# Optimization experiments

Hardware: AMD Instinct MI355X
Metric: run time of the kernel (lower is better)

## Reference

```python
import jax, jax.numpy as jnp
import numpy as np

R = 2  # upsample factor (init kwarg r)


def _cheby1_sos(N, rp, Wn):
    """Pure-numpy replication of scipy.signal.cheby1(N, rp, Wn, 'lowpass', output='sos')
    for even N (all-pole lowpass). Pairing of conjugate poles may differ from scipy's
    zpk2sos ordering but the cascaded transfer function is identical (same poles,
    zeros all at z=-1, same overall gain)."""
    # analog Chebyshev-I prototype (scipy.cheb1ap)
    eps = np.sqrt(10.0 ** (0.1 * rp) - 1.0)
    mu = np.arcsinh(1.0 / eps) / N
    m = np.arange(-N + 1, N, 2)
    theta = np.pi * m / (2.0 * N)
    p = -np.sinh(mu + 1j * theta)
    k = np.prod(-p).real
    if N % 2 == 0:
        k /= np.sqrt(1.0 + eps * eps)
    # pre-warp (fs = 2) and lowpass scale (lp2lp_zpk)
    fs = 2.0
    warped = 2.0 * fs * np.tan(np.pi * Wn / fs)
    p = p * warped
    k = k * warped ** N
    # bilinear transform (bilinear_zpk); zeros -> -1 with multiplicity N
    fs2 = 2.0 * fs
    pz = (fs2 + p) / (fs2 - p)
    kz = k * np.real(1.0 / np.prod(fs2 - p))
    # build SOS: each conjugate pole pair gets two zeros at -1
    pos = pz[np.imag(pz) > 0]  # N//2 poles in upper half plane
    sos = np.zeros((N // 2, 6), dtype=np.float64)
    for i, pp in enumerate(pos):
        sos[i, 0:3] = [1.0, 2.0, 1.0]                      # b: (1 + z^-1)^2
        sos[i, 3:6] = [1.0, -2.0 * pp.real, abs(pp) ** 2]  # a
    sos[0, 0:3] *= kz  # fold overall gain into first section
    return sos


_SOS = _cheby1_sos(8, 0.05, 1.0 / R)  # [4, 6], a0 == 1


def _biquad(x, b0, b1, b2, a1, a2):
    # x: [B, T]; transposed direct-form-II biquad, matching torchaudio's
    def step(carry, xt):
        z1, z2 = carry
        y = b0 * xt + z1
        z1n = b1 * xt - a1 * y + z2
        z2n = b2 * xt - a2 * y
        return (z1n, z2n), y

    B = x.shape[0]
    init = (jnp.zeros((B,), x.dtype), jnp.zeros((B,), x.dtype))
    _, y = jax.lax.scan(step, init, x.T)  # scan over time
    return y.T


def setup_inputs() -> dict:
    key = jax.random.key(0)
    x = jax.random.normal(key, (256, 32768), dtype=jnp.float32)
    return {"x": x}


def reference(x):
    *lead, T = x.shape
    xb = x.reshape(-1, T)
    up = jnp.repeat(xb, R, axis=-1)        # nearest-neighbor upsample by R
    y = up[:, ::-1]                        # flip(-1)
    for row in _SOS:                       # 4 cascaded biquad sections
        b0, b1, b2, a0, a1, a2 = [float(v) for v in row]
        y = _biquad(y, b0 / a0, b1 / a0, b2 / a0, a1 / a0, a2 / a0)
    y = y[:, ::-1]                         # flip back
    return y.reshape(*lead, T * R)
```

## Files before the change

### kernel.cpp

```cpp
#include <hip/hip_runtime.h>
#include <cmath>
#include <complex>


struct KArgs {
  float g;
  float a1[4];
  float a2[4];
  float w[64][8];
};

struct G2 { float4 a, b; };

#define SWZ(q) ((q) ^ ((((q) >> 6) & 7) << 2))

__global__ __launch_bounds__(64)
void cheby_up_kernel(const float* __restrict__ x, float* __restrict__ y, KArgs c) {
  constexpr int T_IN = 32768;
  constexpr int TILE = 2048;
  __shared__ __align__(16) float lbuf[TILE + 64];

  const int row = blockIdx.x >> 4;
  const int tb  = blockIdx.x & 15;
  const int l   = threadIdx.x;
  const float* xrow = x + (size_t)row * T_IN;
  float*       yrow = y + (size_t)row * (size_t)(2 * T_IN);
  const int tbase = TILE * tb;

  const float g = c.g;

  #pragma unroll
  for (int j = 0; j < 8; ++j) {
    int q = 4 * l + 256 * j;
    float4 v = *reinterpret_cast<const float4*>(xrow + tbase + q);
    v.x *= g; v.y *= g; v.z *= g; v.w *= g;
    *reinterpret_cast<float4*>(&lbuf[SWZ(q)]) = v;
  }
  if (l < 16) {
    int q = TILE + 4 * l;
    int gi = tbase + q;
    float4 v = make_float4(0.f, 0.f, 0.f, 0.f);
    if (gi < T_IN) {
      v = *reinterpret_cast<const float4*>(xrow + gi);
      v.x *= g; v.y *= g; v.z *= g; v.w *= g;
    }
    *reinterpret_cast<float4*>(&lbuf[q]) = v;
  }

  auto rd8 = [&](int qq) -> G2 {
    G2 r;
    r.a = *reinterpret_cast<const float4*>(&lbuf[SWZ(qq)]);
    r.b = *reinterpret_cast<const float4*>(&lbuf[SWZ(qq + 4)]);
    return r;
  };

  G2 g3 = rd8(32 * l + 24);
  G2 g2 = rd8(32 * l + 16);
  G2 g1 = rd8(32 * l + 8);
  G2 g0 = rd8(32 * l);

  float ac0=0.f, ac1=0.f, ac2=0.f, ac3=0.f, ac4=0.f, ac5=0.f, ac6=0.f, ac7=0.f;
  #define TAP(jj, xx)                      \
    ac0 = fmaf(c.w[jj][0], (xx), ac0);     \
    ac1 = fmaf(c.w[jj][1], (xx), ac1);     \
    ac2 = fmaf(c.w[jj][2], (xx), ac2);     \
    ac3 = fmaf(c.w[jj][3], (xx), ac3);     \
    ac4 = fmaf(c.w[jj][4], (xx), ac4);     \
    ac5 = fmaf(c.w[jj][5], (xx), ac5);     \
    ac6 = fmaf(c.w[jj][6], (xx), ac6);     \
    ac7 = fmaf(c.w[jj][7], (xx), ac7);
  #pragma unroll
  for (int wg = 0; wg < 8; ++wg) {
    G2 v = rd8(32 * l + 32 + 8 * wg);
    const int j0 = 8 * wg;
    TAP(j0 + 0, v.a.x); TAP(j0 + 1, v.a.y);
    TAP(j0 + 2, v.a.z); TAP(j0 + 3, v.a.w);
    TAP(j0 + 4, v.b.x); TAP(j0 + 5, v.b.y);
    TAP(j0 + 6, v.b.z); TAP(j0 + 7, v.b.w);
  }
  #undef TAP

  const float a10 = c.a1[0], a20 = c.a2[0];
  const float a11 = c.a1[1], a21 = c.a2[1];
  const float a12 = c.a1[2], a22 = c.a2[2];
  const float a13 = c.a1[3], a23 = c.a2[3];

  float z10=ac0, z20=ac1, z11=ac2, z21=ac3;
  float z12=ac4, z22=ac5, z13=ac6, z23=ac7;

  auto step = [&](float x0) -> float {
    float y0 = x0 + z10;
    z10 = fmaf(-a10, y0, fmaf(2.f, x0, z20));
    z20 = fmaf(-a20, y0, x0);
    float y1 = y0 + z11;
    z11 = fmaf(-a11, y1, fmaf(2.f, y0, z21));
    z21 = fmaf(-a21, y1, y0);
    float y2 = y1 + z12;
    z12 = fmaf(-a12, y2, fmaf(2.f, y1, z22));
    z22 = fmaf(-a22, y2, y1);
    float y3 = y2 + z13;
    z13 = fmaf(-a13, y3, fmaf(2.f, y2, z23));
    z23 = fmaf(-a23, y3, y2);
    return y3;
  };

  float o[32];

  auto flush32 = [&](int half) {
    #pragma unroll
    for (int i = 0; i < 8; ++i) {
      int q = 32 * l + 4 * i;
      *reinterpret_cast<float4*>(&lbuf[SWZ(q)]) =
          make_float4(o[4*i], o[4*i+1], o[4*i+2], o[4*i+3]);
    }
    float* yG = yrow + 2 * tbase + half;
    #pragma unroll
    for (int j = 0; j < 8; ++j) {
      int local = 4 * l + 256 * j;
      float4 v = *reinterpret_cast<const float4*>(&lbuf[SWZ(local)]);
      int c64 = local >> 5;
      int m   = local & 31;
      *reinterpret_cast<float4*>(yG + 64 * c64 + m) = v;
    }
  };

  {
    float s;
    s = g3.b.w; o[31] = step(s); o[30] = step(s);
    s = g3.b.z; o[29] = step(s); o[28] = step(s);
    s = g3.b.y; o[27] = step(s); o[26] = step(s);
    s = g3.b.x; o[25] = step(s); o[24] = step(s);
    s = g3.a.w; o[23] = step(s); o[22] = step(s);
    s = g3.a.z; o[21] = step(s); o[20] = step(s);
    s = g3.a.y; o[19] = step(s); o[18] = step(s);
    s = g3.a.x; o[17] = step(s); o[16] = step(s);
    s = g2.b.w; o[15] = step(s); o[14] = step(s);
    s = g2.b.z; o[13] = step(s); o[12] = step(s);
    s = g2.b.y; o[11] = step(s); o[10] = step(s);
    s = g2.b.x; o[9]  = step(s); o[8]  = step(s);
    s = g2.a.w; o[7]  = step(s); o[6]  = step(s);
    s = g2.a.z; o[5]  = step(s); o[4]  = step(s);
    s = g2.a.y; o[3]  = step(s); o[2]  = step(s);
    s = g2.a.x; o[1]  = step(s); o[0]  = step(s);
  }
  flush32(32);

  {
    float s;
    s = g1.b.w; o[31] = step(s); o[30] = step(s);
    s = g1.b.z; o[29] = step(s); o[28] = step(s);
    s = g1.b.y; o[27] = step(s); o[26] = step(s);
    s = g1.b.x; o[25] = step(s); o[24] = step(s);
    s = g1.a.w; o[23] = step(s); o[22] = step(s);
    s = g1.a.z; o[21] = step(s); o[20] = step(s);
    s = g1.a.y; o[19] = step(s); o[18] = step(s);
    s = g1.a.x; o[17] = step(s); o[16] = step(s);
    s = g0.b.w; o[15] = step(s); o[14] = step(s);
    s = g0.b.z; o[13] = step(s); o[12] = step(s);
    s = g0.b.y; o[11] = step(s); o[10] = step(s);
    s = g0.b.x; o[9]  = step(s); o[8]  = step(s);
    s = g0.a.w; o[7]  = step(s); o[6]  = step(s);
    s = g0.a.z; o[5]  = step(s); o[4]  = step(s);
    s = g0.a.y; o[3]  = step(s); o[2]  = step(s);
    s = g0.a.x; o[1]  = step(s); o[0]  = step(s);
  }
  flush32(0);
}


static void step_d(double z[8], double xx, const double A1[4], const double A2[4]) {
  double u = xx;
  double v = u + z[0];
  double n0 = 2.0*u - A1[0]*v + z[1];
  double n1 = u - A2[0]*v;
  u = v; v = u + z[2];
  double n2 = 2.0*u - A1[1]*v + z[3];
  double n3 = u - A2[1]*v;
  u = v; v = u + z[4];
  double n4 = 2.0*u - A1[2]*v + z[5];
  double n5 = u - A2[2]*v;
  u = v; v = u + z[6];
  double n6 = 2.0*u - A1[3]*v + z[7];
  double n7 = u - A2[3]*v;
  z[0]=n0; z[1]=n1; z[2]=n2; z[3]=n3; z[4]=n4; z[5]=n5; z[6]=n6; z[7]=n7;
}

static void matvec8(const double A[8][8], const double v[8], double out[8]) {
  for (int r = 0; r < 8; ++r) {
    double s = 0.0;
    for (int k = 0; k < 8; ++k) s += A[r][k] * v[k];
    out[r] = s;
  }
}

static KArgs compute_args() {
  const int N = 8;
  const double rp = 0.05, Wn = 0.5;
  const double PI = 3.14159265358979323846;
  double eps = std::sqrt(std::pow(10.0, 0.1 * rp) - 1.0);
  double mu = std::asinh(1.0 / eps) / (double)N;
  std::complex<double> p[8];
  std::complex<double> prodNegP(1.0, 0.0);
  int idx = 0;
  for (int m = -N + 1; m < N; m += 2) {
    double theta = PI * (double)m / (2.0 * N);
    std::complex<double> pp = -std::sinh(std::complex<double>(mu, theta));
    p[idx++] = pp;
    prodNegP *= -pp;
  }
  double k = prodNegP.real();
  k /= std::sqrt(1.0 + eps * eps);
  const double fs = 2.0;
  double warped = 2.0 * fs * std::tan(PI * Wn / fs);
  for (int i = 0; i < 8; i++) p[i] *= warped;
  k *= std::pow(warped, (double)N);
  const double fs2 = 2.0 * fs;
  std::complex<double> prodDen(1.0, 0.0);
  for (int i = 0; i < 8; i++) prodDen *= (fs2 - p[i]);
  double kz = k * (1.0 / prodDen).real();

  KArgs c;
  double A1d[4], A2d[4];
  int s = 0;
  for (int i = 0; i < 8; i++) {
    std::complex<double> pz = (fs2 + p[i]) / (fs2 - p[i]);
    if (pz.imag() > 0.0) {
      A1d[s] = -2.0 * pz.real();
      A2d[s] = std::norm(pz);
      c.a1[s] = (float)A1d[s];
      c.a2[s] = (float)A2d[s];
      s++;
    }
  }
  c.g = (float)kz;

  double A[8][8], bv[8];
  for (int i = 0; i < 8; ++i) {
    double z[8] = {0,0,0,0,0,0,0,0};
    z[i] = 1.0;
    step_d(z, 0.0, A1d, A2d);
    for (int r = 0; r < 8; ++r) A[r][i] = z[r];
  }
  {
    double z[8] = {0,0,0,0,0,0,0,0};
    step_d(z, 1.0, A1d, A2d);
    for (int r = 0; r < 8; ++r) bv[r] = z[r];
  }
  double w[8], t[8];
  matvec8(A, bv, t);
  for (int r = 0; r < 8; ++r) w[r] = t[r] + bv[r];
  for (int j = 0; j < 64; ++j) {
    for (int r = 0; r < 8; ++r) c.w[j][r] = (float)w[r];
    matvec8(A, w, t);
    matvec8(A, t, w);
  }
  return c;
}

extern "C" void kernel_launch(void* const* d_in, const int* in_sizes, int n_in,
                              void* d_out, int out_size, void* d_ws, size_t ws_size,
                              hipStream_t stream) {
  const float* x = (const float*)d_in[0];
  float* y = (float*)d_out;
  KArgs c = compute_args();
  int rows = in_sizes[0] / 32768;
  cheby_up_kernel<<<16 * rows, 64, 0, stream>>>(x, y, c);
}
```

Measured before the change: 26.63 us.

## Process two tiles per block and prefetch the next tile during compute

Each block now handles two consecutive 2048-sample tiles instead of one, halving the grid to 2048 blocks. Global loads for the second tile are issued into registers while the first tile's FIR warmup and recurrence run, then staged into LDS afterwards. This aims to hide global load latency inside the block. The cost is fewer blocks for latency hiding across the GPU and more live registers per thread, which may lower occupancy.

```diff
diff --git a/kernel.cpp b/kernel.cpp
--- a/kernel.cpp
+++ b/kernel.cpp
@@ -20,151 +20,172 @@
   constexpr int TILE = 2048;
   __shared__ __align__(16) float lbuf[TILE + 64];
 
-  const int row = blockIdx.x >> 4;
-  const int tb  = blockIdx.x & 15;
+  const int row = blockIdx.x >> 3;
+  const int pr  = blockIdx.x & 7;
   const int l   = threadIdx.x;
   const float* xrow = x + (size_t)row * T_IN;
   float*       yrow = y + (size_t)row * (size_t)(2 * T_IN);
-  const int tbase = TILE * tb;
 
   const float g = c.g;
-
-  #pragma unroll
-  for (int j = 0; j < 8; ++j) {
-    int q = 4 * l + 256 * j;
-    float4 v = *reinterpret_cast<const float4*>(xrow + tbase + q);
-    v.x *= g; v.y *= g; v.z *= g; v.w *= g;
-    *reinterpret_cast<float4*>(&lbuf[SWZ(q)]) = v;
-  }
-  if (l < 16) {
-    int q = TILE + 4 * l;
-    int gi = tbase + q;
-    float4 v = make_float4(0.f, 0.f, 0.f, 0.f);
-    if (gi < T_IN) {
-      v = *reinterpret_cast<const float4*>(xrow + gi);
-      v.x *= g; v.y *= g; v.z *= g; v.w *= g;
-    }
-    *reinterpret_cast<float4*>(&lbuf[q]) = v;
-  }
-
-  auto rd8 = [&](int qq) -> G2 {
-    G2 r;
-    r.a = *reinterpret_cast<const float4*>(&lbuf[SWZ(qq)]);
-    r.b = *reinterpret_cast<const float4*>(&lbuf[SWZ(qq + 4)]);
-    return r;
-  };
-
-  G2 g3 = rd8(32 * l + 24);
-  G2 g2 = rd8(32 * l + 16);
-  G2 g1 = rd8(32 * l + 8);
-  G2 g0 = rd8(32 * l);
-
-  float ac0=0.f, ac1=0.f, ac2=0.f, ac3=0.f, ac4=0.f, ac5=0.f, ac6=0.f, ac7=0.f;
-  #define TAP(jj, xx)                      \
-    ac0 = fmaf(c.w[jj][0], (xx), ac0);     \
-    ac1 = fmaf(c.w[jj][1], (xx), ac1);     \
-    ac2 = fmaf(c.w[jj][2], (xx), ac2);     \
-    ac3 = fmaf(c.w[jj][3], (xx), ac3);     \
-    ac4 = fmaf(c.w[jj][4], (xx), ac4);     \
-    ac5 = fmaf(c.w[jj][5], (xx), ac5);     \
-    ac6 = fmaf(c.w[jj][6], (xx), ac6);     \
-    ac7 = fmaf(c.w[jj][7], (xx), ac7);
-  #pragma unroll
-  for (int wg = 0; wg < 8; ++wg) {
-    G2 v = rd8(32 * l + 32 + 8 * wg);
-    const int j0 = 8 * wg;
-    TAP(j0 + 0, v.a.x); TAP(j0 + 1, v.a.y);
-    TAP(j0 + 2, v.a.z); TAP(j0 + 3, v.a.w);
-    TAP(j0 + 4, v.b.x); TAP(j0 + 5, v.b.y);
-    TAP(j0 + 6, v.b.z); TAP(j0 + 7, v.b.w);
-  }
-  #undef TAP
-
   const float a10 = c.a1[0], a20 = c.a2[0];
   const float a11 = c.a1[1], a21 = c.a2[1];
   const float a12 = c.a1[2], a22 = c.a2[2];
   const float a13 = c.a1[3], a23 = c.a2[3];
 
-  float z10=ac0, z20=ac1, z11=ac2, z21=ac3;
-  float z12=ac4, z22=ac5, z13=ac6, z23=ac7;
-
-  auto step = [&](float x0) -> float {
-    float y0 = x0 + z10;
-    z10 = fmaf(-a10, y0, fmaf(2.f, x0, z20));
-    z20 = fmaf(-a20, y0, x0);
-    float y1 = y0 + z11;
-    z11 = fmaf(-a11, y1, fmaf(2.f, y0, z21));
-    z21 = fmaf(-a21, y1, y0);
-    float y2 = y1 + z12;
-    z12 = fmaf(-a12, y2, fmaf(2.f, y1, z22));
-    z22 = fmaf(-a22, y2, y1);
-    float y3 = y2 + z13;
-    z13 = fmaf(-a13, y3, fmaf(2.f, y2, z23));
-    z23 = fmaf(-a23, y3, y2);
-    return y3;
-  };
-
-  float o[32];
-
-  auto flush32 = [&](int half) {
+  float4 r[8];
+  float4 h;
+
+  auto issue_loads = [&](int tb) {
+    const float* src = xrow + TILE * tb;
     #pragma unroll
-    for (int i = 0; i < 8; ++i) {
-      int q = 32 * l + 4 * i;
-      *reinterpret_cast<float4*>(&lbuf[SWZ(q)]) =
-          make_float4(o[4*i], o[4*i+1], o[4*i+2], o[4*i+3]);
-    }
-    float* yG = yrow + 2 * tbase + half;
+    for (int j = 0; j < 8; ++j)
+      r[j] = *reinterpret_cast<const float4*>(src + 4 * l + 256 * j);
+    h = make_float4(0.f, 0.f, 0.f, 0.f);
+    const int gi = TILE * (tb + 1) + 4 * l;
+    if (l < 16 && gi < T_IN)
+      h = *reinterpret_cast<const float4*>(xrow + gi);
+  };
+
+  auto write_stage = [&]() {
     #pragma unroll
     for (int j = 0; j < 8; ++j) {
-      int local = 4 * l + 256 * j;
-      float4 v = *reinterpret_cast<const float4*>(&lbuf[SWZ(local)]);
-      int c64 = local >> 5;
-      int m   = local & 31;
-      *reinterpret_cast<float4*>(yG + 64 * c64 + m) = v;
-    }
-  };
-
-  {
-    float s;
-    s = g3.b.w; o[31] = step(s); o[30] = step(s);
-    s = g3.b.z; o[29] = step(s); o[28] = step(s);
-    s = g3.b.y; o[27] = step(s); o[26] = step(s);
-    s = g3.b.x; o[25] = step(s); o[24] = step(s);
-    s = g3.a.w; o[23] = step(s); o[22] = step(s);
-    s = g3.a.z; o[21] = step(s); o[20] = step(s);
-    s = g3.a.y; o[19] = step(s); o[18] = step(s);
-    s = g3.a.x; o[17] = step(s); o[16] = step(s);
-    s = g2.b.w; o[15] = step(s); o[14] = step(s);
-    s = g2.b.z; o[13] = step(s); o[12] = step(s);
-    s = g2.b.y; o[11] = step(s); o[10] = step(s);
-    s = g2.b.x; o[9]  = step(s); o[8]  = step(s);
-    s = g2.a.w; o[7]  = step(s); o[6]  = step(s);
-    s = g2.a.z; o[5]  = step(s); o[4]  = step(s);
-    s = g2.a.y; o[3]  = step(s); o[2]  = step(s);
-    s = g2.a.x; o[1]  = step(s); o[0]  = step(s);
-  }
-  flush32(32);
-
-  {
-    float s;
-    s = g1.b.w; o[31] = step(s); o[30] = step(s);
-    s = g1.b.z; o[29] = step(s); o[28] = step(s);
-    s = g1.b.y; o[27] = step(s); o[26] = step(s);
-    s = g1.b.x; o[25] = step(s); o[24] = step(s);
-    s = g1.a.w; o[23] = step(s); o[22] = step(s);
-    s = g1.a.z; o[21] = step(s); o[20] = step(s);
-    s = g1.a.y; o[19] = step(s); o[18] = step(s);
-    s = g1.a.x; o[17] = step(s); o[16] = step(s);
-    s = g0.b.w; o[15] = step(s); o[14] = step(s);
-    s = g0.b.z; o[13] = step(s); o[12] = step(s);
-    s = g0.b.y; o[11] = step(s); o[10] = step(s);
-    s = g0.b.x; o[9]  = step(s); o[8]  = step(s);
-    s = g0.a.w; o[7]  = step(s); o[6]  = step(s);
-    s = g0.a.z; o[5]  = step(s); o[4]  = step(s);
-    s = g0.a.y; o[3]  = step(s); o[2]  = step(s);
-    s = g0.a.x; o[1]  = step(s); o[0]  = step(s);
-  }
-  flush32(0);
+      const int q = 4 * l + 256 * j;
+      float4 v = r[j];
+      v.x *= g; v.y *= g; v.z *= g; v.w *= g;
+      *reinterpret_cast<float4*>(&lbuf[SWZ(q)]) = v;
+    }
+    if (l < 16) {
+      float4 v = h;
+      v.x *= g; v.y *= g; v.z *= g; v.w *= g;
+      *reinterpret_cast<float4*>(&lbuf[TILE + 4 * l]) = v;
+    }
+  };
+
+  auto rd8 = [&](int qq) -> G2 {
+    G2 v;
+    v.a = *reinterpret_cast<const float4*>(&lbuf[SWZ(qq)]);
+    v.b = *reinterpret_cast<const float4*>(&lbuf[SWZ(qq + 4)]);
+    return v;
+  };
+
+  auto process_tile = [&](int tb, int nxt) {
+    G2 g3 = rd8(32 * l + 24);
+    G2 g2 = rd8(32 * l + 16);
+    G2 g1 = rd8(32 * l + 8);
+    G2 g0 = rd8(32 * l);
+
+    if (nxt >= 0) issue_loads(nxt);
+
+    float ac0=0.f, ac1=0.f, ac2=0.f, ac3=0.f, ac4=0.f, ac5=0.f, ac6=0.f, ac7=0.f;
+    #define TAP(jj, xx)                      \
+      ac0 = fmaf(c.w[jj][0], (xx), ac0);     \
+      ac1 = fmaf(c.w[jj][1], (xx), ac1);     \
+      ac2 = fmaf(c.w[jj][2], (xx), ac2);     \
+      ac3 = fmaf(c.w[jj][3], (xx), ac3);     \
+      ac4 = fmaf(c.w[jj][4], (xx), ac4);     \
+      ac5 = fmaf(c.w[jj][5], (xx), ac5);     \
+      ac6 = fmaf(c.w[jj][6], (xx), ac6);     \
+      ac7 = fmaf(c.w[jj][7], (xx), ac7);
+    #pragma unroll
+    for (int wg = 0; wg < 8; ++wg) {
+      G2 v = rd8(32 * l + 32 + 8 * wg);
+      const int j0 = 8 * wg;
+      TAP(j0 + 0, v.a.x); TAP(j0 + 1, v.a.y);
+      TAP(j0 + 2, v.a.z); TAP(j0 + 3, v.a.w);
+      TAP(j0 + 4, v.b.x); TAP(j0 + 5, v.b.y);
+      TAP(j0 + 6, v.b.z); TAP(j0 + 7, v.b.w);
+    }
+    #undef TAP
+
+    float z10=ac0, z20=ac1, z11=ac2, z21=ac3;
+    float z12=ac4, z22=ac5, z13=ac6, z23=ac7;
+
+    auto step = [&](float x0) -> float {
+      float y0 = x0 + z10;
+      z10 = fmaf(-a10, y0, fmaf(2.f, x0, z20));
+      z20 = fmaf(-a20, y0, x0);
+      float y1 = y0 + z11;
+      z11 = fmaf(-a11, y1, fmaf(2.f, y0, z21));
+      z21 = fmaf(-a21, y1, y0);
+      float y2 = y1 + z12;
+      z12 = fmaf(-a12, y2, fmaf(2.f, y1, z22));
+      z22 = fmaf(-a22, y2, y1);
+      float y3 = y2 + z13;
+      z13 = fmaf(-a13, y3, fmaf(2.f, y2, z23));
+      z23 = fmaf(-a23, y3, y2);
+      return y3;
+    };
+
+    float o[32];
+
+    auto flush32 = [&](int half) {
+      #pragma unroll
+      for (int i = 0; i < 8; ++i) {
+        int q = 32 * l + 4 * i;
+        *reinterpret_cast<float4*>(&lbuf[SWZ(q)]) =
+            make_float4(o[4*i], o[4*i+1], o[4*i+2], o[4*i+3]);
+      }
+      float* yG = yrow + 2 * TILE * tb + half;
+      #pragma unroll
+      for (int j = 0; j < 8; ++j) {
+        int local = 4 * l + 256 * j;
+        float4 v = *reinterpret_cast<const float4*>(&lbuf[SWZ(local)]);
+        int c64 = local >> 5;
+        int m   = local & 31;
+        *reinterpret_cast<float4*>(yG + 64 * c64 + m) = v;
+      }
+    };
+
+    {
+      float s;
+      s = g3.b.w; o[31] = step(s); o[30] = step(s);
+      s = g3.b.z; o[29] = step(s); o[28] = step(s);
+      s = g3.b.y; o[27] = step(s); o[26] = step(s);
+      s = g3.b.x; o[25] = step(s); o[24] = step(s);
+      s = g3.a.w; o[23] = step(s); o[22] = step(s);
+      s = g3.a.z; o[21] = step(s); o[20] = step(s);
+      s = g3.a.y; o[19] = step(s); o[18] = step(s);
+      s = g3.a.x; o[17] = step(s); o[16] = step(s);
+      s = g2.b.w; o[15] = step(s); o[14] = step(s);
+      s = g2.b.z; o[13] = step(s); o[12] = step(s);
+      s = g2.b.y; o[11] = step(s); o[10] = step(s);
+      s = g2.b.x; o[9]  = step(s); o[8]  = step(s);
+      s = g2.a.w; o[7]  = step(s); o[6]  = step(s);
+      s = g2.a.z; o[5]  = step(s); o[4]  = step(s);
+      s = g2.a.y; o[3]  = step(s); o[2]  = step(s);
+      s = g2.a.x; o[1]  = step(s); o[0]  = step(s);
+    }
+    flush32(32);
+
+    {
+      float s;
+      s = g1.b.w; o[31] = step(s); o[30] = step(s);
+      s = g1.b.z; o[29] = step(s); o[28] = step(s);
+      s = g1.b.y; o[27] = step(s); o[26] = step(s);
+      s = g1.b.x; o[25] = step(s); o[24] = step(s);
+      s = g1.a.w; o[23] = step(s); o[22] = step(s);
+      s = g1.a.z; o[21] = step(s); o[20] = step(s);
+      s = g1.a.y; o[19] = step(s); o[18] = step(s);
+      s = g1.a.x; o[17] = step(s); o[16] = step(s);
+      s = g0.b.w; o[15] = step(s); o[14] = step(s);
+      s = g0.b.z; o[13] = step(s); o[12] = step(s);
+      s = g0.b.y; o[11] = step(s); o[10] = step(s);
+      s = g0.b.x; o[9]  = step(s); o[8]  = step(s);
+      s = g0.a.w; o[7]  = step(s); o[6]  = step(s);
+      s = g0.a.z; o[5]  = step(s); o[4]  = step(s);
+      s = g0.a.y; o[3]  = step(s); o[2]  = step(s);
+      s = g0.a.x; o[1]  = step(s); o[0]  = step(s);
+    }
+    flush32(0);
+
+    if (nxt >= 0) write_stage();
+  };
+
+  const int tb0 = 2 * pr;
+  issue_loads(tb0);
+  write_stage();
+  process_tile(tb0, tb0 + 1);
+  process_tile(tb0 + 1, -1);
 }
 
 
@@ -264,5 +285,5 @@
   float* y = (float*)d_out;
   KArgs c = compute_args();
   int rows = in_sizes[0] / 32768;
-  cheby_up_kernel<<<16 * rows, 64, 0, stream>>>(x, y, c);
-}
+  cheby_up_kernel<<<8 * rows, 64, 0, stream>>>(x, y, c);
+}
```

After: 37.78 us. +41.9%, slower.
